# Optimization experiments

Measured on AMD Instinct MI355X. Metric: run time of the kernel, lower is better.

Reference implementation:

```python
import jax, jax.numpy as jnp
import numpy as np
import math

B, S, D = 16, 4096, 64

def setup_inputs() -> dict:
    key = jax.random.key(0)
    kq, kk, kv = jax.random.split(key, 3)
    query = jax.random.normal(kq, (B, S, D), dtype=jnp.float32)
    k_ = jax.random.normal(kk, (B, S, D), dtype=jnp.float32)
    value = jax.random.normal(kv, (B, S, D), dtype=jnp.float32)
    # causal mask: 1 = allowed, 0 = masked (set to -inf), broadcast over batch
    mask = jnp.tril(jnp.ones((S, S), dtype=jnp.int32))[None, :, :]
    return {"query": query, "key": k_, "value": value, "mask": mask, "key_dim": D}

def reference(query, key, value, mask, key_dim):
    # scores: [B, S, S] = Q @ K^T / sqrt(dk)
    scores = jnp.einsum('bqd,bkd->bqk', query, key) / math.sqrt(key_dim)
    scores = jnp.where(mask == 0, -jnp.inf, scores)
    attn = jax.nn.softmax(scores, axis=-1)
    return jnp.einsum('bqk,bkd->bqd', attn, value)
```

## Files before the change

kernel.cpp:

```cpp
#include <hip/hip_runtime.h>

typedef _Float16 half8 __attribute__((ext_vector_type(8)));
typedef float f32x4 __attribute__((ext_vector_type(4)));

union Frag { half8 v; unsigned int u32[4]; uint4 u4; };
union Pack4 { _Float16 h[4]; uint2 u; };

constexpr int S = 4096;
constexpr int D = 64;
constexpr int NB = 16;
constexpr int LTS = 72;

__global__ __launch_bounds__(256)
void prep_kernel(const float* __restrict__ K, const float* __restrict__ V,
                 _Float16* __restrict__ K16, _Float16* __restrict__ VT) {
    __shared__ float tl[64 * 66];
    const int tid = threadIdx.x;
    const int s0 = blockIdx.x * 64;
    const int b  = blockIdx.y;
    const float* Kb = K + ((size_t)b * S + s0) * D;
    const float* Vb = V + ((size_t)b * S + s0) * D;
    _Float16* K16b = K16 + ((size_t)b * S + s0) * D;

    #pragma unroll
    for (int i = 0; i < 2; ++i) {
        int e8 = tid + 256 * i;
        float4 a = ((const float4*)Kb)[2 * e8];
        float4 c = ((const float4*)Kb)[2 * e8 + 1];
        Frag f;
        f.v[0]=(_Float16)a.x; f.v[1]=(_Float16)a.y; f.v[2]=(_Float16)a.z; f.v[3]=(_Float16)a.w;
        f.v[4]=(_Float16)c.x; f.v[5]=(_Float16)c.y; f.v[6]=(_Float16)c.z; f.v[7]=(_Float16)c.w;
        ((uint4*)K16b)[e8] = f.u4;
    }
    #pragma unroll
    for (int i = 0; i < 4; ++i) {
        int fi = tid + 256 * i;
        int r = fi >> 4, c4 = (fi & 15) << 2;
        float4 v = *(const float4*)(Vb + (size_t)r * D + c4);
        float2* p = (float2*)&tl[r * 66 + c4];
        p[0] = make_float2(v.x, v.y);
        p[1] = make_float2(v.z, v.w);
    }
    __syncthreads();
    _Float16* VTb = VT + (size_t)b * D * S;
    #pragma unroll
    for (int i = 0; i < 2; ++i) {
        int fi = tid + 256 * i;
        int d = fi >> 3, s8 = (fi & 7) << 3;
        Frag f;
        #pragma unroll
        for (int j = 0; j < 8; ++j) f.v[j] = (_Float16)tl[(s8 + j) * 66 + d];
        *(uint4*)(VTb + (size_t)d * S + s0 + s8) = f.u4;
    }
}

template <int SPLIT>
__device__ __forceinline__
void fattn_body(const float* __restrict__ Q, const _Float16* __restrict__ K16,
                const _Float16* __restrict__ VT16, float* __restrict__ Out,
                _Float16* __restrict__ OP, float* __restrict__ LP,
                int b, int J, int t0, int t1, int h) {
    __shared__ __align__(16) _Float16 kt[64 * LTS];
    __shared__ __align__(16) _Float16 vt[64 * LTS];
    __shared__ __align__(16) _Float16 pt[4 * 32 * LTS];

    const int tid  = threadIdx.x;
    const int wave = tid >> 6;
    const int lane = tid & 63;
    const int ln   = lane & 15;
    const int quad = lane >> 4;

    const float* Qb = Q + (size_t)b * S * D;
    const _Float16* Kb = K16 + (size_t)b * S * D;
    const _Float16* VTb = VT16 + (size_t)b * D * S;

    const float qscale = 0.125f * 1.44269504088896340736f;
    const int qrow_base = J * 128 + wave * 32;
    const int tw = (qrow_base + 31) >> 6;

    Frag qf[2][2];
    #pragma unroll
    for (int qg = 0; qg < 2; ++qg) {
        const float* qrow = Qb + (size_t)(qrow_base + qg * 16 + ln) * D + quad * 8;
        #pragma unroll
        for (int ks = 0; ks < 2; ++ks) {
            float4 a = *(const float4*)(qrow + ks * 32);
            float4 c = *(const float4*)(qrow + ks * 32 + 4);
            Frag f;
            f.v[0]=(_Float16)(a.x*qscale); f.v[1]=(_Float16)(a.y*qscale);
            f.v[2]=(_Float16)(a.z*qscale); f.v[3]=(_Float16)(a.w*qscale);
            f.v[4]=(_Float16)(c.x*qscale); f.v[5]=(_Float16)(c.y*qscale);
            f.v[6]=(_Float16)(c.z*qscale); f.v[7]=(_Float16)(c.w*qscale);
            qf[qg][ks] = f;
        }
    }

    f32x4 o[2][4] = {};
    float l_acc[2] = {0.f, 0.f};
    _Float16* ptw = pt + wave * 32 * LTS;

    for (int t = t0; t < t1; ++t) {
        const int k0 = t * 64;
        __syncthreads();

        #pragma unroll
        for (int i = 0; i < 2; ++i) {
            int fi = tid + 256 * i;
            int r = fi >> 3, c8 = (fi & 7) << 3;
            uint4 kk = *(const uint4*)(Kb + (size_t)(k0 + r) * D + c8);
            uint4 vv = *(const uint4*)(VTb + (size_t)r * S + k0 + c8);
            *(uint4*)(kt + r * LTS + c8) = kk;
            *(uint4*)(vt + r * LTS + c8) = vv;
        }
        __syncthreads();

        #pragma unroll
        for (int ct = 0; ct < 4; ++ct) {
            Frag kf0, kf1;
            kf0.u4 = *(const uint4*)(kt + (ct * 16 + ln) * LTS + quad * 8);
            kf1.u4 = *(const uint4*)(kt + (ct * 16 + ln) * LTS + 32 + quad * 8);
            #pragma unroll
            for (int qg = 0; qg < 2; ++qg) {
                f32x4 acc = {0.f, 0.f, 0.f, 0.f};
                acc = __builtin_amdgcn_mfma_f32_16x16x32_f16(kf0.v, qf[qg][0].v, acc, 0, 0, 0);
                acc = __builtin_amdgcn_mfma_f32_16x16x32_f16(kf1.v, qf[qg][1].v, acc, 0, 0, 0);
                if (t >= tw) {
                    int keyb = k0 + ct * 16 + quad * 4;
                    int qrow = qrow_base + qg * 16 + ln;
                    #pragma unroll
                    for (int r = 0; r < 4; ++r)
                        if (keyb + r > qrow) acc[r] = -1e30f;
                }
                Pack4 pk;
                float psum = 0.f;
                #pragma unroll
                for (int r = 0; r < 4; ++r) {
                    float p = exp2f(acc[r]);
                    psum += p;
                    pk.h[r] = (_Float16)p;
                }
                l_acc[qg] += psum;
                *(uint2*)(ptw + (qg * 16 + ln) * LTS + ct * 16 + quad * 4) = pk.u;
            }
        }

        Frag pf[2][2];
        #pragma unroll
        for (int qg = 0; qg < 2; ++qg)
            #pragma unroll
            for (int ks = 0; ks < 2; ++ks)
                pf[qg][ks].u4 = *(const uint4*)(ptw + (qg * 16 + ln) * LTS + ks * 32 + quad * 8);

        #pragma unroll
        for (int ks = 0; ks < 2; ++ks) {
            #pragma unroll
            for (int sub = 0; sub < 4; ++sub) {
                Frag vf;
                vf.u4 = *(const uint4*)(vt + (sub * 16 + ln) * LTS + ks * 32 + quad * 8);
                #pragma unroll
                for (int qg = 0; qg < 2; ++qg)
                    o[qg][sub] = __builtin_amdgcn_mfma_f32_16x16x32_f16(pf[qg][ks].v, vf.v, o[qg][sub], 0, 0, 0);
            }
        }
    }

    float lf[2];
    #pragma unroll
    for (int qg = 0; qg < 2; ++qg) {
        float x = l_acc[qg];
        x += __shfl_xor(x, 16, 64);
        x += __shfl_xor(x, 32, 64);
        lf[qg] = x;
    }

    if (SPLIT) {
        _Float16* OPb = OP + (size_t)(((b * 32 + J) * 4 + h)) * 8192;
        float* LPb = LP + (size_t)(((b * 32 + J) * 4 + h)) * 128;
        #pragma unroll
        for (int qg = 0; qg < 2; ++qg) {
            if (quad == 0) LPb[wave * 32 + qg * 16 + ln] = lf[qg];
            #pragma unroll
            for (int r = 0; r < 4; ++r) {
                float lrow = __shfl(lf[qg], quad * 4 + r, 64);
                float inv = (lrow > 0.f) ? (1.0f / lrow) : 0.f;
                #pragma unroll
                for (int sub = 0; sub < 4; ++sub)
                    OPb[(wave * 32 + qg * 16 + quad * 4 + r) * 64 + sub * 16 + ln] =
                        (_Float16)(o[qg][sub][r] * inv);
            }
        }
    } else {
        float* Ob = Out + (size_t)b * S * D;
        #pragma unroll
        for (int qg = 0; qg < 2; ++qg) {
            #pragma unroll
            for (int r = 0; r < 4; ++r) {
                float lrow = __shfl(lf[qg], quad * 4 + r, 64);
                float inv = 1.0f / lrow;
                #pragma unroll
                for (int sub = 0; sub < 4; ++sub)
                    Ob[(size_t)(qrow_base + qg * 16 + quad * 4 + r) * D + sub * 16 + ln] =
                        o[qg][sub][r] * inv;
            }
        }
    }
}

__global__ __launch_bounds__(256, 4)
void fattn_split_kernel(const float* __restrict__ Q, const _Float16* __restrict__ K16,
                        const _Float16* __restrict__ VT16,
                        _Float16* __restrict__ OP, float* __restrict__ LP) {
    const int bx = blockIdx.x;
    const int J = 31 - (bx >> 6);
    const int h = (bx >> 4) & 3;
    const int b = bx & 15;
    const int n  = 2 * J + 2;
    const int t0 = (h * n) >> 2;
    const int t1 = ((h + 1) * n) >> 2;
    fattn_body<1>(Q, K16, VT16, nullptr, OP, LP, b, J, t0, t1, h);
}

__global__ __launch_bounds__(256, 4)
void fattn_kernel(const float* __restrict__ Q, const _Float16* __restrict__ K16,
                  const _Float16* __restrict__ VT16, float* __restrict__ Out) {
    const int bx = blockIdx.x;
    const int J = 31 - (bx >> 4);
    const int b = bx & 15;
    fattn_body<0>(Q, K16, VT16, Out, nullptr, nullptr, b, J, 0, 2 * J + 2, 0);
}

__global__ __launch_bounds__(256)
void reduce_kernel(const _Float16* __restrict__ OP, const float* __restrict__ LP,
                   float* __restrict__ Out) {
    const int rb = blockIdx.x;
    const int b  = rb & 15;
    const int J  = rb >> 4;
    const int tid = threadIdx.x;
    const _Float16* p = OP + (size_t)(b * 32 + J) * 4 * 8192;
    const float* l = LP + (size_t)(b * 32 + J) * 4 * 128;
    float* Ob = Out + (size_t)b * S * D + (size_t)J * 8192;
    #pragma unroll
    for (int i = 0; i < 4; ++i) {
        int e8 = tid + 256 * i;
        int q  = e8 >> 3;
        float lw[4], lsum = 0.f;
        #pragma unroll
        for (int hh = 0; hh < 4; ++hh) { lw[hh] = l[hh * 128 + q]; lsum += lw[hh]; }
        float inv = 1.0f / lsum;
        float acc[8] = {};
        #pragma unroll
        for (int hh = 0; hh < 4; ++hh) {
            half8 v = *(const half8*)(p + (size_t)hh * 8192 + e8 * 8);
            #pragma unroll
            for (int j = 0; j < 8; ++j) acc[j] += lw[hh] * (float)v[j];
        }
        float4 r0, r1;
        r0.x = acc[0]*inv; r0.y = acc[1]*inv; r0.z = acc[2]*inv; r0.w = acc[3]*inv;
        r1.x = acc[4]*inv; r1.y = acc[5]*inv; r1.z = acc[6]*inv; r1.w = acc[7]*inv;
        ((float4*)Ob)[2 * e8]     = r0;
        ((float4*)Ob)[2 * e8 + 1] = r1;
    }
}

extern "C" void kernel_launch(void* const* d_in, const int* in_sizes, int n_in,
                              void* d_out, int out_size, void* d_ws, size_t ws_size,
                              hipStream_t stream) {
    const float* Q = (const float*)d_in[0];
    const float* K = (const float*)d_in[1];
    const float* V = (const float*)d_in[2];
    float* O = (float*)d_out;

    const size_t prepBytes = (size_t)NB * S * D * 2;
    _Float16* K16  = (_Float16*)d_ws;
    _Float16* VT16 = (_Float16*)((char*)d_ws + prepBytes);

    const size_t opOff = 2 * prepBytes;
    const size_t opBytes = (size_t)NB * 32 * 4 * 8192 * 2;
    const size_t lpOff = opOff + opBytes;
    const size_t lpBytes = (size_t)NB * 32 * 4 * 128 * 4;
    const size_t need = lpOff + lpBytes;

    hipLaunchKernelGGL(prep_kernel, dim3(S / 64, NB), dim3(256), 0, stream, K, V, K16, VT16);

    if (ws_size >= need) {
        _Float16* OP = (_Float16*)((char*)d_ws + opOff);
        float* LP = (float*)((char*)d_ws + lpOff);
        hipLaunchKernelGGL(fattn_split_kernel, dim3(128 * NB), dim3(256), 0, stream,
                           Q, K16, VT16, OP, LP);
        hipLaunchKernelGGL(reduce_kernel, dim3(32 * NB), dim3(256), 0, stream, OP, LP, O);
    } else {
        hipLaunchKernelGGL(fattn_kernel, dim3(32 * NB), dim3(256), 0, stream, Q, K16, VT16, O);
    }
}
```

Baseline: 199.5 us.

## Keep P tile in registers via permlane swaps instead of LDS round trip

The softmax probabilities are no longer written to shared memory and reloaded as MFMA A-operands. They are repacked in registers with v_permlane32/16_swap so the S-fragment layout matches the PV MFMA input layout, and the pt LDS buffer is removed. This frees LDS, and launch bounds are raised from 4 to 6 blocks per SM so more waves can be resident. exp2f is replaced by the raw hardware exp2 builtin. The risk is register pressure under the tighter launch bound, which could cause spills.

```diff
diff --git a/kernel.cpp b/kernel.cpp
--- a/kernel.cpp
+++ b/kernel.cpp
@@ -4,12 +4,20 @@
 typedef float f32x4 __attribute__((ext_vector_type(4)));
 
 union Frag { half8 v; unsigned int u32[4]; uint4 u4; };
-union Pack4 { _Float16 h[4]; uint2 u; };
+union Pack4 { _Float16 h[4]; unsigned int u[2]; };
 
 constexpr int S = 4096;
 constexpr int D = 64;
 constexpr int NB = 16;
 constexpr int LTS = 72;
+
+__device__ __forceinline__ float ex2(float x) {
+#if __has_builtin(__builtin_amdgcn_exp2f)
+    return __builtin_amdgcn_exp2f(x);
+#else
+    return exp2f(x);
+#endif
+}
 
 __global__ __launch_bounds__(256)
 void prep_kernel(const float* __restrict__ K, const float* __restrict__ V,
@@ -62,11 +70,10 @@
                 int b, int J, int t0, int t1, int h) {
     __shared__ __align__(16) _Float16 kt[64 * LTS];
     __shared__ __align__(16) _Float16 vt[64 * LTS];
-    __shared__ __align__(16) _Float16 pt[4 * 32 * LTS];
 
     const int tid  = threadIdx.x;
+    const int lane = tid & 63;
     const int wave = tid >> 6;
-    const int lane = tid & 63;
     const int ln   = lane & 15;
     const int quad = lane >> 4;
 
@@ -97,7 +104,6 @@
 
     f32x4 o[2][4] = {};
     float l_acc[2] = {0.f, 0.f};
-    _Float16* ptw = pt + wave * 32 * LTS;
 
     for (int t = t0; t < t1; ++t) {
         const int k0 = t * 64;
@@ -115,51 +121,57 @@
         __syncthreads();
 
         #pragma unroll
-        for (int ct = 0; ct < 4; ++ct) {
-            Frag kf0, kf1;
-            kf0.u4 = *(const uint4*)(kt + (ct * 16 + ln) * LTS + quad * 8);
-            kf1.u4 = *(const uint4*)(kt + (ct * 16 + ln) * LTS + 32 + quad * 8);
+        for (int ks = 0; ks < 2; ++ks) {
+            unsigned w[2][2][2];
+            #pragma unroll
+            for (int cl = 0; cl < 2; ++cl) {
+                const int ct = ks * 2 + cl;
+                Frag kf0, kf1;
+                kf0.u4 = *(const uint4*)(kt + (ct * 16 + ln) * LTS + quad * 8);
+                kf1.u4 = *(const uint4*)(kt + (ct * 16 + ln) * LTS + 32 + quad * 8);
+                #pragma unroll
+                for (int qg = 0; qg < 2; ++qg) {
+                    f32x4 acc = {0.f, 0.f, 0.f, 0.f};
+                    acc = __builtin_amdgcn_mfma_f32_16x16x32_f16(kf0.v, qf[qg][0].v, acc, 0, 0, 0);
+                    acc = __builtin_amdgcn_mfma_f32_16x16x32_f16(kf1.v, qf[qg][1].v, acc, 0, 0, 0);
+                    if (t >= tw) {
+                        int keyb = k0 + ct * 16 + quad * 4;
+                        int qrow = qrow_base + qg * 16 + ln;
+                        #pragma unroll
+                        for (int r = 0; r < 4; ++r)
+                            if (keyb + r > qrow) acc[r] = -1e30f;
+                    }
+                    float p0 = ex2(acc[0]), p1 = ex2(acc[1]);
+                    float p2 = ex2(acc[2]), p3 = ex2(acc[3]);
+                    l_acc[qg] += (p0 + p1) + (p2 + p3);
+                    Pack4 pk;
+                    pk.h[0] = (_Float16)p0; pk.h[1] = (_Float16)p1;
+                    pk.h[2] = (_Float16)p2; pk.h[3] = (_Float16)p3;
+                    w[qg][cl][0] = pk.u[0];
+                    w[qg][cl][1] = pk.u[1];
+                }
+            }
+
+            Frag pf[2];
             #pragma unroll
             for (int qg = 0; qg < 2; ++qg) {
-                f32x4 acc = {0.f, 0.f, 0.f, 0.f};
-                acc = __builtin_amdgcn_mfma_f32_16x16x32_f16(kf0.v, qf[qg][0].v, acc, 0, 0, 0);
-                acc = __builtin_amdgcn_mfma_f32_16x16x32_f16(kf1.v, qf[qg][1].v, acc, 0, 0, 0);
-                if (t >= tw) {
-                    int keyb = k0 + ct * 16 + quad * 4;
-                    int qrow = qrow_base + qg * 16 + ln;
-                    #pragma unroll
-                    for (int r = 0; r < 4; ++r)
-                        if (keyb + r > qrow) acc[r] = -1e30f;
-                }
-                Pack4 pk;
-                float psum = 0.f;
-                #pragma unroll
-                for (int r = 0; r < 4; ++r) {
-                    float p = exp2f(acc[r]);
-                    psum += p;
-                    pk.h[r] = (_Float16)p;
-                }
-                l_acc[qg] += psum;
-                *(uint2*)(ptw + (qg * 16 + ln) * LTS + ct * 16 + quad * 4) = pk.u;
-            }
-        }
-
-        Frag pf[2][2];
-        #pragma unroll
-        for (int qg = 0; qg < 2; ++qg)
-            #pragma unroll
-            for (int ks = 0; ks < 2; ++ks)
-                pf[qg][ks].u4 = *(const uint4*)(ptw + (qg * 16 + ln) * LTS + ks * 32 + quad * 8);
-
-        #pragma unroll
-        for (int ks = 0; ks < 2; ++ks) {
+                unsigned x0 = w[qg][0][0], y0 = w[qg][1][0];
+                unsigned x1 = w[qg][0][1], y1 = w[qg][1][1];
+                asm("v_permlane32_swap_b32 %0, %1" : "+v"(x0), "+v"(y0));
+                asm("v_permlane32_swap_b32 %0, %1" : "+v"(x1), "+v"(y1));
+                asm("v_permlane16_swap_b32 %0, %1" : "+v"(x0), "+v"(y0));
+                asm("v_permlane16_swap_b32 %0, %1" : "+v"(x1), "+v"(y1));
+                pf[qg].u32[0] = x0; pf[qg].u32[1] = x1;
+                pf[qg].u32[2] = y0; pf[qg].u32[3] = y1;
+            }
+
             #pragma unroll
             for (int sub = 0; sub < 4; ++sub) {
                 Frag vf;
                 vf.u4 = *(const uint4*)(vt + (sub * 16 + ln) * LTS + ks * 32 + quad * 8);
                 #pragma unroll
                 for (int qg = 0; qg < 2; ++qg)
-                    o[qg][sub] = __builtin_amdgcn_mfma_f32_16x16x32_f16(pf[qg][ks].v, vf.v, o[qg][sub], 0, 0, 0);
+                    o[qg][sub] = __builtin_amdgcn_mfma_f32_16x16x32_f16(pf[qg].v, vf.v, o[qg][sub], 0, 0, 0);
             }
         }
     }
@@ -206,7 +218,7 @@
     }
 }
 
-__global__ __launch_bounds__(256, 4)
+__global__ __launch_bounds__(256, 6)
 void fattn_split_kernel(const float* __restrict__ Q, const _Float16* __restrict__ K16,
                         const _Float16* __restrict__ VT16,
                         _Float16* __restrict__ OP, float* __restrict__ LP) {
@@ -220,7 +232,7 @@
     fattn_body<1>(Q, K16, VT16, nullptr, OP, LP, b, J, t0, t1, h);
 }
 
-__global__ __launch_bounds__(256, 4)
+__global__ __launch_bounds__(256, 6)
 void fattn_kernel(const float* __restrict__ Q, const _Float16* __restrict__ K16,
                   const _Float16* __restrict__ VT16, float* __restrict__ Out) {
     const int bx = blockIdx.x;
```

New measurement: 347.3 us. +74.1%, slower.
